# Optimization experiments

Hardware: AMD Instinct MI355X
Metric: run time of the kernel (lower is better)

Reference implementation:

```python
import jax, jax.numpy as jnp
import numpy as np

TAU = 0.1
SIGMA = 0.2
EPS = 1e-08
NUM_BINS = 128
IN_FEATURES = 512
OUT_FEATURES = 128
N = 4096
C = 16


def setup_inputs() -> dict:
    key = jax.random.key(0)
    ks = jax.random.split(key, 8)
    x1 = jax.random.normal(ks[0], (N, IN_FEATURES), dtype=jnp.float32)
    x2 = jax.random.normal(ks[1], (N, IN_FEATURES), dtype=jnp.float32)
    y1 = jax.random.randint(ks[2], (N,), 0, C, dtype=jnp.int32)
    y2 = jax.random.randint(ks[3], (N,), 0, C, dtype=jnp.int32)
    W1 = jax.random.normal(ks[4], (IN_FEATURES, OUT_FEATURES), dtype=jnp.float32) * 0.02
    b1 = jnp.zeros((OUT_FEATURES,), dtype=jnp.float32)
    W2 = jax.random.normal(ks[5], (OUT_FEATURES, OUT_FEATURES), dtype=jnp.float32) * 0.02
    b2 = jnp.zeros((OUT_FEATURES,), dtype=jnp.float32)
    bins = jnp.linspace(-5.0, 5.0, NUM_BINS).astype(jnp.float32)
    return {"input_embeddings_1": x1, "y1": y1, "input_embeddings_2": x2, "y2": y2,
            "W1": W1, "b1": b1, "W2": W2, "b2": b2, "bins": bins, "num_classes": C}


def _marginal_pdf(x_norm, bins):
    # x_norm: (b, D) L2-normalized rows; bins: (num_bins,)
    # residuals: (b, D, num_bins) -- dominant memory-bound intermediate
    kernel = jnp.exp(-0.5 * ((x_norm[:, :, None] - bins[None, None, :]) / SIGMA) ** 2)
    pdf = kernel.mean(axis=1)                         # (b, num_bins)
    pdf = pdf / (pdf.sum(axis=1, keepdims=True) + EPS)
    return jax.nn.softmax(pdf, axis=-1)


def _get_distribution(x, y, bins, num_classes):
    # x: (b, out_features) projected embeddings
    x_norm = x / jnp.linalg.norm(x, axis=1, keepdims=True)
    pdf = _marginal_pdf(x_norm, bins)                 # (b, num_bins)
    sums = jax.ops.segment_sum(pdf, y, num_segments=num_classes)
    counts = jax.ops.segment_sum(jnp.ones((y.shape[0],), pdf.dtype), y, num_segments=num_classes)
    return sums / counts[:, None]                     # (C, num_bins) per-class mean pdf


def _kld_matrix(A, M):
    P = jnp.concatenate([A, M], axis=0)               # (2C, num_bins)
    logP = jnp.log(P)
    inter = jnp.sum(P[:, None, :] * (logP[:, None, :] - logP[None, :, :]), axis=-1)
    n = P.shape[0]
    return inter * (1.0 - jnp.eye(n, dtype=P.dtype))


def reference(input_embeddings_1, y1, input_embeddings_2, y2, W1, b1, W2, b2, bins, num_classes):
    def proj(x):
        h = jax.nn.relu(x @ W1 + b1)
        return h @ W2 + b2

    dA = _get_distribution(proj(input_embeddings_1), y1, bins, num_classes)
    dB = _get_distribution(proj(input_embeddings_2), y2, bins, num_classes)
    M = 0.5 * (dA + dB)
    J = 0.5 * (_kld_matrix(dA, M) + _kld_matrix(dB, M))  # (2C, 2C)
    div_ij = jnp.diagonal(J, offset=num_classes)
    div_ji = jnp.diagonal(J, offset=-num_classes)
    positives = jnp.concatenate([div_ij, div_ji], axis=0)
    nominator = jnp.exp(positives / TAU)
    denominator = jnp.sum(jnp.exp(J / TAU), axis=1)
    partial_loss = -jnp.log(nominator / denominator)
    return jnp.mean(partial_loss)
```

## Files before the change

### kernel.cpp

```cpp
#include <hip/hip_runtime.h>
#include <hip/hip_bf16.h>

#define NROWS 4096
#define IN_F 512
#define OUT_F 128
#define NBINS 128
#define NCLS 16
#define EPSV 1e-8f
#define TAUV 0.1f
#define PSTRIDE (NCLS * NBINS + 32)

#define C2EXP (-18.0336880f)
#define INV_STEP (12.7f)
#define WRAD 17

#if defined(__has_builtin)
#if __has_builtin(__builtin_amdgcn_exp2f)
#define EXP2F(x) __builtin_amdgcn_exp2f(x)
#else
#define EXP2F(x) exp2f(x)
#endif
#else
#define EXP2F(x) exp2f(x)
#endif

typedef __attribute__((ext_vector_type(8))) short bf16x8;
typedef __attribute__((ext_vector_type(4))) float f32x4;

__device__ __forceinline__ short cvt_bf16(float x) {
    __hip_bfloat16 h = __float2bfloat16(x);
    return *reinterpret_cast<short*>(&h);
}

__global__ __launch_bounds__(128) void prep_w(
    const float* __restrict__ W1, const float* __restrict__ W2,
    __hip_bfloat16* __restrict__ W1T, __hip_bfloat16* __restrict__ W2T)
{
    const int n = blockIdx.x;
    const int t = threadIdx.x;
    for (int k = t; k < IN_F; k += 128)
        W1T[(size_t)n * IN_F + k] = __float2bfloat16(W1[(size_t)k * OUT_F + n]);
    W2T[(size_t)n * OUT_F + t] = __float2bfloat16(W2[(size_t)t * OUT_F + n]);
}

__global__ __launch_bounds__(512) void fused_proj_pdf(
    const float* __restrict__ X1, const float* __restrict__ X2,
    const int* __restrict__ Y1, const int* __restrict__ Y2,
    const __hip_bfloat16* __restrict__ W1T, const float* __restrict__ b1,
    const __hip_bfloat16* __restrict__ W2T, const float* __restrict__ b2,
    const float* __restrict__ bins,
    float* __restrict__ partial, float* __restrict__ pcnt)
{
    __shared__ __hip_bfloat16 xb[16][IN_F + 8];
    __shared__ __hip_bfloat16 h_lds[16][136];
    __shared__ float pout[16][128];
    __shared__ float rowX[8][2][128];
    __shared__ float smrows[16][128];
    __shared__ float bins_s[NBINS];
    __shared__ int   labs[16];
    const int tid  = threadIdx.x;
    const int wave = tid >> 6;
    const int lane = tid & 63;
    const int lr   = lane & 15;
    const int kg   = lane >> 4;
    const int row0 = blockIdx.x * 16;
    const int batch = (row0 < NROWS) ? 0 : 1;
    const float* __restrict__ X = batch ? X2 : X1;
    const int* __restrict__ Y = batch ? Y2 : Y1;
    const int xr0 = batch ? row0 - NROWS : row0;
    const int col = wave * 16 + lr;

    if (tid < NBINS) bins_s[tid] = bins[tid];
    if (tid >= 128 && tid < 144) labs[tid - 128] = Y[xr0 + tid - 128];

    for (int i = tid; i < 16 * 128; i += 512) {
        const int r = i >> 7, c4 = i & 127;
        float4 v = *reinterpret_cast<const float4*>(
            X + (size_t)(xr0 + r) * IN_F + c4 * 4);
        short4 s;
        s.x = cvt_bf16(v.x); s.y = cvt_bf16(v.y);
        s.z = cvt_bf16(v.z); s.w = cvt_bf16(v.w);
        *reinterpret_cast<short4*>(&xb[r][c4 * 4]) = s;
    }
    __syncthreads();

    f32x4 acc = {0.f, 0.f, 0.f, 0.f};
    {
        const __hip_bfloat16* __restrict__ wrow = W1T + (size_t)col * IN_F;
        #pragma unroll 4
        for (int ks = 0; ks < IN_F / 32; ++ks) {
            const int kb = ks * 32 + kg * 8;
            bf16x8 a = *reinterpret_cast<const bf16x8*>(&xb[lr][kb]);
            bf16x8 b = *reinterpret_cast<const bf16x8*>(wrow + kb);
            acc = __builtin_amdgcn_mfma_f32_16x16x32_bf16(a, b, acc, 0, 0, 0);
        }
    }
    {
        const float bb = b1[col];
        #pragma unroll
        for (int q = 0; q < 4; ++q)
            h_lds[kg * 4 + q][col] = __float2bfloat16(fmaxf(acc[q] + bb, 0.f));
    }
    __syncthreads();

    f32x4 c2 = {0.f, 0.f, 0.f, 0.f};
    {
        const __hip_bfloat16* __restrict__ w2row = W2T + (size_t)col * OUT_F;
        #pragma unroll
        for (int ks = 0; ks < OUT_F / 32; ++ks) {
            const int kb = ks * 32 + kg * 8;
            bf16x8 a2 = *reinterpret_cast<const bf16x8*>(&h_lds[lr][kb]);
            bf16x8 b2f = *reinterpret_cast<const bf16x8*>(w2row + kb);
            c2 = __builtin_amdgcn_mfma_f32_16x16x32_bf16(a2, b2f, c2, 0, 0, 0);
        }
    }
    {
        const float cb = b2[col];
        #pragma unroll
        for (int q = 0; q < 4; ++q)
            pout[kg * 4 + q][col] = c2[q] + cb;
    }
    __syncthreads();

    const int m0 = wave * 2, m1 = m0 + 1;

    const float p00 = pout[m0][lane], p01 = pout[m0][lane + 64];
    const float p10 = pout[m1][lane], p11 = pout[m1][lane + 64];

    float s0 = p00 * p00 + p01 * p01;
    float s1 = p10 * p10 + p11 * p11;
    #pragma unroll
    for (int off = 32; off; off >>= 1) {
        s0 += __shfl_xor(s0, off);
        s1 += __shfl_xor(s1, off);
    }
    const float i0 = __frsqrt_rn(s0), i1 = __frsqrt_rn(s1);
    const float x00 = p00 * i0, x01 = p01 * i0;
    const float x10 = p10 * i1, x11 = p11 * i1;

    rowX[wave][0][lane]      = x00;
    rowX[wave][0][lane + 64] = x01;
    rowX[wave][1][lane]      = x10;
    rowX[wave][1][lane + 64] = x11;

    float xlo = fminf(fminf(x00, x01), fminf(x10, x11));
    float xhi = fmaxf(fmaxf(x00, x01), fmaxf(x10, x11));
    #pragma unroll
    for (int off = 32; off; off >>= 1) {
        xlo = fminf(xlo, __shfl_xor(xlo, off));
        xhi = fmaxf(xhi, __shfl_xor(xhi, off));
    }
    int imin = (int)floorf((xlo + 5.0f) * INV_STEP) - WRAD;
    int imax = (int)ceilf ((xhi + 5.0f) * INV_STEP) + WRAD;
    imin = imin < 0 ? 0 : (imin > 127 ? 127 : imin);
    imax = imax > 127 ? 127 : (imax < 0 ? 0 : imax);
    if (imax > imin + 63) imax = imin + 63;
    const int nact = imax - imin + 1;
    const int j = imin + lane;
    const bool act = (j <= imax);
    const float bj = bins_s[act ? j : imax];

    const float4* __restrict__ x0v = reinterpret_cast<const float4*>(&rowX[wave][0][0]);
    const float4* __restrict__ x1v = reinterpret_cast<const float4*>(&rowX[wave][1][0]);
    float aA0 = 0.f, aA1 = 0.f, aB0 = 0.f, aB1 = 0.f;
    #pragma unroll 4
    for (int q = 0; q < 32; ++q) {
        float4 u = x0v[q];
        float4 v = x1v[q];
        float t;
        t = u.x - bj; aA0 += EXP2F((C2EXP * t) * t);
        t = u.z - bj; aA1 += EXP2F((C2EXP * t) * t);
        t = v.x - bj; aB0 += EXP2F((C2EXP * t) * t);
        t = v.z - bj; aB1 += EXP2F((C2EXP * t) * t);
        t = u.y - bj; aA0 += EXP2F((C2EXP * t) * t);
        t = u.w - bj; aA1 += EXP2F((C2EXP * t) * t);
        t = v.y - bj; aB0 += EXP2F((C2EXP * t) * t);
        t = v.w - bj; aB1 += EXP2F((C2EXP * t) * t);
    }
    float pdf0 = act ? (aA0 + aA1) * (1.0f / OUT_F) : 0.f;
    float pdf1 = act ? (aB0 + aB1) * (1.0f / OUT_F) : 0.f;

    float t0 = pdf0, t1 = pdf1;
    #pragma unroll
    for (int off = 32; off; off >>= 1) {
        t0 += __shfl_xor(t0, off);
        t1 += __shfl_xor(t1, off);
    }
    pdf0 *= 1.0f / (t0 + EPSV);
    pdf1 *= 1.0f / (t1 + EPSV);

    float mx0 = pdf0, mx1 = pdf1;
    #pragma unroll
    for (int off = 32; off; off >>= 1) {
        mx0 = fmaxf(mx0, __shfl_xor(mx0, off));
        mx1 = fmaxf(mx1, __shfl_xor(mx1, off));
    }
    const float q0 = act ? __expf(pdf0 - mx0) : 0.f;
    const float q1 = act ? __expf(pdf1 - mx1) : 0.f;
    const float ez0 = __expf(-mx0), ez1 = __expf(-mx1);
    float es0 = q0, es1 = q1;
    #pragma unroll
    for (int off = 32; off; off >>= 1) {
        es0 += __shfl_xor(es0, off);
        es1 += __shfl_xor(es1, off);
    }
    es0 += (float)(NBINS - nact) * ez0;
    es1 += (float)(NBINS - nact) * ez1;
    const float r0 = 1.0f / es0, r1 = 1.0f / es1;
    const float z0 = ez0 * r0, z1 = ez1 * r1;

    const int sa = lane - imin;
    const int sb = lane + 64 - imin;
    const float w0a = __shfl(q0, sa & 63) * r0;
    const float w0b = __shfl(q0, sb & 63) * r0;
    const float w1a = __shfl(q1, sa & 63) * r1;
    const float w1b = __shfl(q1, sb & 63) * r1;
    const bool ina = (unsigned)sa < (unsigned)nact;
    const bool inb = (unsigned)sb < (unsigned)nact;

    smrows[m0][lane]      = ina ? w0a : z0;
    smrows[m0][lane + 64] = inb ? w0b : z0;
    smrows[m1][lane]      = ina ? w1a : z1;
    smrows[m1][lane + 64] = inb ? w1b : z1;
    __syncthreads();

    {
        const int c_cls = tid >> 5;
        const int jq    = tid & 31;
        f32x4 accp = {0.f, 0.f, 0.f, 0.f};
        int ccnt = 0;
        #pragma unroll 4
        for (int r = 0; r < 16; ++r) {
            const float4 v = *reinterpret_cast<const float4*>(&smrows[r][jq * 4]);
            const float h = (labs[r] == c_cls) ? 1.f : 0.f;
            accp.x = fmaf(h, v.x, accp.x);
            accp.y = fmaf(h, v.y, accp.y);
            accp.z = fmaf(h, v.z, accp.z);
            accp.w = fmaf(h, v.w, accp.w);
            ccnt += (labs[r] == c_cls);
        }
        *reinterpret_cast<f32x4*>(
            &partial[(size_t)blockIdx.x * PSTRIDE + c_cls * NBINS + jq * 4]) = accp;
        if (jq == 0) pcnt[(size_t)blockIdx.x * NCLS + c_cls] = (float)ccnt;
    }
}

__global__ __launch_bounds__(256) void merge_kernel(
    const float* __restrict__ partial, const float* __restrict__ pcnt,
    float* __restrict__ dist, float* __restrict__ cntg)
{
    __shared__ float sd[16][17];
    __shared__ float sc[4];
    const int b = blockIdx.x;
    const int bc = b >> 3, jg = b & 7;
    const int batch = bc >> 4, c = bc & 15;
    const int j0 = jg * 16;
    const int tid = threadIdx.x;
    const int jl = tid & 15, s = tid >> 4;

    float acc = 0.f;
    #pragma unroll 4
    for (int k = 0; k < 16; ++k) {
        const int sb = s + k * 16;
        acc += partial[(size_t)(batch * 256 + sb) * PSTRIDE + c * NBINS + j0 + jl];
    }
    sd[s][jl] = acc;

    float cv = pcnt[(size_t)(batch * 256 + tid) * NCLS + c];
    #pragma unroll
    for (int off = 32; off; off >>= 1) cv += __shfl_xor(cv, off);
    if ((tid & 63) == 0) sc[tid >> 6] = cv;
    __syncthreads();

    if (tid < 16) {
        float d = 0.f;
        #pragma unroll
        for (int q = 0; q < 16; ++q) d += sd[q][tid];
        dist[(size_t)bc * NBINS + j0 + tid] = d;
    }
    if (jg == 0 && tid == 0) cntg[bc] = sc[0] + sc[1] + sc[2] + sc[3];
}

__global__ __launch_bounds__(512) void final_kernel(
    const float* __restrict__ dist, const float* __restrict__ cntg,
    float* __restrict__ out)
{
    __shared__ float P_A[32][132], L_A[32][132];
    __shared__ float P_B[32][132], L_B[32][132];
    __shared__ float JA[32][32], JB[32][32];
    __shared__ float pls[32];
    __shared__ float cnt[32];
    __shared__ float HA[32], HB[32];
    const int tid = threadIdx.x;

    if (tid < 32) cnt[tid] = cntg[tid];
    __syncthreads();

    for (int s = tid; s < NCLS * NBINS; s += 512) {
        const int c = s >> 7, jj = s & 127;
        const float a = dist[(size_t)c * NBINS + jj] / cnt[c];
        const float b = dist[(size_t)(16 + c) * NBINS + jj] / cnt[16 + c];
        const float mm = 0.5f * (a + b);
        const float lm = __logf(mm);
        P_A[c][jj] = a;        L_A[c][jj] = __logf(a);
        P_A[c + 16][jj] = mm;  L_A[c + 16][jj] = lm;
        P_B[c][jj] = b;        L_B[c][jj] = __logf(b);
        P_B[c + 16][jj] = mm;  L_B[c + 16][jj] = lm;
    }
    __syncthreads();

    if (tid < 64) {
        const int i = tid & 31;
        const float4* Pv = reinterpret_cast<const float4*>(
            (tid < 32) ? &P_A[i][0] : &P_B[i][0]);
        const float4* Lv = reinterpret_cast<const float4*>(
            (tid < 32) ? &L_A[i][0] : &L_B[i][0]);
        float h = 0.f;
        #pragma unroll 4
        for (int q = 0; q < 32; ++q) {
            float4 p = Pv[q], l = Lv[q];
            h = fmaf(p.x, l.x, h); h = fmaf(p.y, l.y, h);
            h = fmaf(p.z, l.z, h); h = fmaf(p.w, l.w, h);
        }
        if (tid < 32) HA[i] = h; else HB[i] = h;
    }
    __syncthreads();

    if (tid < 128) {
        const int side = tid >> 6;
        const int t = tid & 63;
        const int i0 = (t >> 3) << 2, k0 = (t & 7) << 2;
        const float4* pr[4];
        const float4* lq[4];
        #pragma unroll
        for (int a = 0; a < 4; ++a) {
            pr[a] = reinterpret_cast<const float4*>(
                side ? &P_B[i0 + a][0] : &P_A[i0 + a][0]);
            lq[a] = reinterpret_cast<const float4*>(
                side ? &L_B[k0 + a][0] : &L_A[k0 + a][0]);
        }
        float accv[4][4];
        #pragma unroll
        for (int a = 0; a < 4; ++a)
            #pragma unroll
            for (int b = 0; b < 4; ++b) accv[a][b] = 0.f;
        for (int q = 0; q < 32; ++q) {
            float4 Pv[4], Lv[4];
            #pragma unroll
            for (int a = 0; a < 4; ++a) { Pv[a] = pr[a][q]; Lv[a] = lq[a][q]; }
            #pragma unroll
            for (int a = 0; a < 4; ++a)
                #pragma unroll
                for (int b = 0; b < 4; ++b) {
                    accv[a][b] = fmaf(Pv[a].x, Lv[b].x, accv[a][b]);
                    accv[a][b] = fmaf(Pv[a].y, Lv[b].y, accv[a][b]);
                    accv[a][b] = fmaf(Pv[a].z, Lv[b].z, accv[a][b]);
                    accv[a][b] = fmaf(Pv[a].w, Lv[b].w, accv[a][b]);
                }
        }
        float (*Jout)[32] = side ? JB : JA;
        #pragma unroll
        for (int a = 0; a < 4; ++a)
            #pragma unroll
            for (int b = 0; b < 4; ++b)
                Jout[i0 + a][k0 + b] = accv[a][b];
    }
    __syncthreads();

    for (int p = tid; p < 32 * 32; p += 512) {
        const int i = p >> 5, k = p & 31;
        const float Jv = (i == k) ? 0.f
            : 0.5f * ((HA[i] - JA[i][k]) + (HB[i] - JB[i][k]));
        JA[i][k] = Jv;
    }
    __syncthreads();

    if (tid < 32) {
        float den = 0.f;
        for (int k = 0; k < 32; ++k) den += __expf(JA[tid][k] * (1.0f / TAUV));
        const float pos = JA[tid][(tid + 16) & 31];
        pls[tid] = -(pos * (1.0f / TAUV)) + __logf(den);
    }
    __syncthreads();
    if (tid == 0) {
        float s = 0.f;
        for (int i = 0; i < 32; ++i) s += pls[i];
        out[0] = s * (1.0f / 32.0f);
    }
}

extern "C" void kernel_launch(void* const* d_in, const int* in_sizes, int n_in,
                              void* d_out, int out_size, void* d_ws, size_t ws_size,
                              hipStream_t stream)
{
    const float* x1   = (const float*)d_in[0];
    const int*   y1   = (const int*)d_in[1];
    const float* x2   = (const float*)d_in[2];
    const int*   y2   = (const int*)d_in[3];
    const float* W1   = (const float*)d_in[4];
    const float* b1   = (const float*)d_in[5];
    const float* W2   = (const float*)d_in[6];
    const float* b2   = (const float*)d_in[7];
    const float* bins = (const float*)d_in[8];
    float* out = (float*)d_out;

    char* ws = (char*)d_ws;
    float* partial = (float*)ws;
    float* pcnt    = partial + (size_t)512 * PSTRIDE;
    float* dist    = pcnt + 512 * NCLS;
    float* cntg    = dist + 32 * NBINS;
    __hip_bfloat16* W1T = (__hip_bfloat16*)(cntg + 64);
    __hip_bfloat16* W2T = W1T + (size_t)OUT_F * IN_F;

    prep_w<<<128, 128, 0, stream>>>(W1, W2, W1T, W2T);
    fused_proj_pdf<<<512, 512, 0, stream>>>(x1, x2, y1, y2, W1T, b1, W2T, b2,
                                            bins, partial, pcnt);
    merge_kernel<<<256, 256, 0, stream>>>(partial, pcnt, dist, cntg);
    final_kernel<<<1, 512, 0, stream>>>(dist, cntg, out);
}
```

Baseline: 47.56 us.

## Halve rows per block to double grid size and process one row per wave

Each fused projection/pdf block now handles 8 rows instead of 16, so 1024 blocks are launched and each wave computes the KDE histogram for a single row. MFMA tiles still cover 16 rows, so half of each MFMA's work is duplicated and discarded. The merge kernel is reshaped to reduce twice as many partial histograms, and the workspace grows accordingly. The aim is more parallelism and shorter per-block latency on the large CU count, at the cost of doubling W1/W2 reads across blocks and doubling the partial-sum traffic.

After: 56.83 us, median of 2. 19.5% more time.

```diff
diff --git a/kernel.cpp b/kernel.cpp
--- a/kernel.cpp
+++ b/kernel.cpp
@@ -51,29 +51,30 @@
     const float* __restrict__ bins,
     float* __restrict__ partial, float* __restrict__ pcnt)
 {
-    __shared__ __hip_bfloat16 xb[16][IN_F + 8];
-    __shared__ __hip_bfloat16 h_lds[16][136];
-    __shared__ float pout[16][128];
-    __shared__ float rowX[8][2][128];
-    __shared__ float smrows[16][128];
+    __shared__ __hip_bfloat16 xb[8][IN_F + 8];
+    __shared__ __hip_bfloat16 h_lds[8][136];
+    __shared__ float pout[8][128];
+    __shared__ float rowX[8][128];
+    __shared__ float smrows[8][128];
     __shared__ float bins_s[NBINS];
-    __shared__ int   labs[16];
+    __shared__ int   labs[8];
     const int tid  = threadIdx.x;
     const int wave = tid >> 6;
     const int lane = tid & 63;
     const int lr   = lane & 15;
     const int kg   = lane >> 4;
-    const int row0 = blockIdx.x * 16;
+    const int row0 = blockIdx.x * 8;
     const int batch = (row0 < NROWS) ? 0 : 1;
     const float* __restrict__ X = batch ? X2 : X1;
     const int* __restrict__ Y = batch ? Y2 : Y1;
-    const int xr0 = batch ? row0 - NROWS : row0;
+    const int xr0 = row0 & (NROWS - 1);
     const int col = wave * 16 + lr;
 
     if (tid < NBINS) bins_s[tid] = bins[tid];
-    if (tid >= 128 && tid < 144) labs[tid - 128] = Y[xr0 + tid - 128];
-
-    for (int i = tid; i < 16 * 128; i += 512) {
+    if (tid >= 128 && tid < 136) labs[tid - 128] = Y[xr0 + tid - 128];
+
+    #pragma unroll
+    for (int i = tid; i < 8 * 128; i += 512) {
         const int r = i >> 7, c4 = i & 127;
         float4 v = *reinterpret_cast<const float4*>(
             X + (size_t)(xr0 + r) * IN_F + c4 * 4);
@@ -90,7 +91,7 @@
         #pragma unroll 4
         for (int ks = 0; ks < IN_F / 32; ++ks) {
             const int kb = ks * 32 + kg * 8;
-            bf16x8 a = *reinterpret_cast<const bf16x8*>(&xb[lr][kb]);
+            bf16x8 a = *reinterpret_cast<const bf16x8*>(&xb[lr & 7][kb]);
             bf16x8 b = *reinterpret_cast<const bf16x8*>(wrow + kb);
             acc = __builtin_amdgcn_mfma_f32_16x16x32_bf16(a, b, acc, 0, 0, 0);
         }
@@ -98,8 +99,11 @@
     {
         const float bb = b1[col];
         #pragma unroll
-        for (int q = 0; q < 4; ++q)
-            h_lds[kg * 4 + q][col] = __float2bfloat16(fmaxf(acc[q] + bb, 0.f));
+        for (int q = 0; q < 4; ++q) {
+            const int m = kg * 4 + q;
+            if (m < 8)
+                h_lds[m][col] = __float2bfloat16(fmaxf(acc[q] + bb, 0.f));
+        }
     }
     __syncthreads();
 
@@ -109,7 +113,7 @@
         #pragma unroll
         for (int ks = 0; ks < OUT_F / 32; ++ks) {
             const int kb = ks * 32 + kg * 8;
-            bf16x8 a2 = *reinterpret_cast<const bf16x8*>(&h_lds[lr][kb]);
+            bf16x8 a2 = *reinterpret_cast<const bf16x8*>(&h_lds[lr & 7][kb]);
             bf16x8 b2f = *reinterpret_cast<const bf16x8*>(w2row + kb);
             c2 = __builtin_amdgcn_mfma_f32_16x16x32_bf16(a2, b2f, c2, 0, 0, 0);
         }
@@ -117,34 +121,29 @@
     {
         const float cb = b2[col];
         #pragma unroll
-        for (int q = 0; q < 4; ++q)
-            pout[kg * 4 + q][col] = c2[q] + cb;
-    }
-    __syncthreads();
-
-    const int m0 = wave * 2, m1 = m0 + 1;
-
-    const float p00 = pout[m0][lane], p01 = pout[m0][lane + 64];
-    const float p10 = pout[m1][lane], p11 = pout[m1][lane + 64];
-
-    float s0 = p00 * p00 + p01 * p01;
-    float s1 = p10 * p10 + p11 * p11;
-    #pragma unroll
-    for (int off = 32; off; off >>= 1) {
-        s0 += __shfl_xor(s0, off);
-        s1 += __shfl_xor(s1, off);
-    }
-    const float i0 = __frsqrt_rn(s0), i1 = __frsqrt_rn(s1);
-    const float x00 = p00 * i0, x01 = p01 * i0;
-    const float x10 = p10 * i1, x11 = p11 * i1;
-
-    rowX[wave][0][lane]      = x00;
-    rowX[wave][0][lane + 64] = x01;
-    rowX[wave][1][lane]      = x10;
-    rowX[wave][1][lane + 64] = x11;
-
-    float xlo = fminf(fminf(x00, x01), fminf(x10, x11));
-    float xhi = fmaxf(fmaxf(x00, x01), fmaxf(x10, x11));
+        for (int q = 0; q < 4; ++q) {
+            const int m = kg * 4 + q;
+            if (m < 8)
+                pout[m][col] = c2[q] + cb;
+        }
+    }
+    __syncthreads();
+
+    const int m = wave;
+
+    const float p0 = pout[m][lane], p1 = pout[m][lane + 64];
+
+    float ss = p0 * p0 + p1 * p1;
+    #pragma unroll
+    for (int off = 32; off; off >>= 1) ss += __shfl_xor(ss, off);
+    const float inv = __frsqrt_rn(ss);
+    const float x0 = p0 * inv, x1 = p1 * inv;
+
+    rowX[m][lane]      = x0;
+    rowX[m][lane + 64] = x1;
+
+    float xlo = fminf(x0, x1);
+    float xhi = fmaxf(x0, x1);
     #pragma unroll
     for (int off = 32; off; off >>= 1) {
         xlo = fminf(xlo, __shfl_xor(xlo, off));
@@ -160,68 +159,45 @@
     const bool act = (j <= imax);
     const float bj = bins_s[act ? j : imax];
 
-    const float4* __restrict__ x0v = reinterpret_cast<const float4*>(&rowX[wave][0][0]);
-    const float4* __restrict__ x1v = reinterpret_cast<const float4*>(&rowX[wave][1][0]);
-    float aA0 = 0.f, aA1 = 0.f, aB0 = 0.f, aB1 = 0.f;
+    const float4* __restrict__ xv = reinterpret_cast<const float4*>(&rowX[m][0]);
+    float a0 = 0.f, a1 = 0.f;
     #pragma unroll 4
     for (int q = 0; q < 32; ++q) {
-        float4 u = x0v[q];
-        float4 v = x1v[q];
+        float4 u = xv[q];
         float t;
-        t = u.x - bj; aA0 += EXP2F((C2EXP * t) * t);
-        t = u.z - bj; aA1 += EXP2F((C2EXP * t) * t);
-        t = v.x - bj; aB0 += EXP2F((C2EXP * t) * t);
-        t = v.z - bj; aB1 += EXP2F((C2EXP * t) * t);
-        t = u.y - bj; aA0 += EXP2F((C2EXP * t) * t);
-        t = u.w - bj; aA1 += EXP2F((C2EXP * t) * t);
-        t = v.y - bj; aB0 += EXP2F((C2EXP * t) * t);
-        t = v.w - bj; aB1 += EXP2F((C2EXP * t) * t);
-    }
-    float pdf0 = act ? (aA0 + aA1) * (1.0f / OUT_F) : 0.f;
-    float pdf1 = act ? (aB0 + aB1) * (1.0f / OUT_F) : 0.f;
-
-    float t0 = pdf0, t1 = pdf1;
-    #pragma unroll
-    for (int off = 32; off; off >>= 1) {
-        t0 += __shfl_xor(t0, off);
-        t1 += __shfl_xor(t1, off);
-    }
-    pdf0 *= 1.0f / (t0 + EPSV);
-    pdf1 *= 1.0f / (t1 + EPSV);
-
-    float mx0 = pdf0, mx1 = pdf1;
-    #pragma unroll
-    for (int off = 32; off; off >>= 1) {
-        mx0 = fmaxf(mx0, __shfl_xor(mx0, off));
-        mx1 = fmaxf(mx1, __shfl_xor(mx1, off));
-    }
-    const float q0 = act ? __expf(pdf0 - mx0) : 0.f;
-    const float q1 = act ? __expf(pdf1 - mx1) : 0.f;
-    const float ez0 = __expf(-mx0), ez1 = __expf(-mx1);
-    float es0 = q0, es1 = q1;
-    #pragma unroll
-    for (int off = 32; off; off >>= 1) {
-        es0 += __shfl_xor(es0, off);
-        es1 += __shfl_xor(es1, off);
-    }
-    es0 += (float)(NBINS - nact) * ez0;
-    es1 += (float)(NBINS - nact) * ez1;
-    const float r0 = 1.0f / es0, r1 = 1.0f / es1;
-    const float z0 = ez0 * r0, z1 = ez1 * r1;
+        t = u.x - bj; a0 += EXP2F((C2EXP * t) * t);
+        t = u.z - bj; a1 += EXP2F((C2EXP * t) * t);
+        t = u.y - bj; a0 += EXP2F((C2EXP * t) * t);
+        t = u.w - bj; a1 += EXP2F((C2EXP * t) * t);
+    }
+    float pdf = act ? (a0 + a1) * (1.0f / OUT_F) : 0.f;
+
+    float ts = pdf;
+    #pragma unroll
+    for (int off = 32; off; off >>= 1) ts += __shfl_xor(ts, off);
+    pdf *= 1.0f / (ts + EPSV);
+
+    float mx = pdf;
+    #pragma unroll
+    for (int off = 32; off; off >>= 1) mx = fmaxf(mx, __shfl_xor(mx, off));
+    const float qv = act ? __expf(pdf - mx) : 0.f;
+    const float ez = __expf(-mx);
+    float es = qv;
+    #pragma unroll
+    for (int off = 32; off; off >>= 1) es += __shfl_xor(es, off);
+    es += (float)(NBINS - nact) * ez;
+    const float rcp = 1.0f / es;
+    const float z = ez * rcp;
 
     const int sa = lane - imin;
     const int sb = lane + 64 - imin;
-    const float w0a = __shfl(q0, sa & 63) * r0;
-    const float w0b = __shfl(q0, sb & 63) * r0;
-    const float w1a = __shfl(q1, sa & 63) * r1;
-    const float w1b = __shfl(q1, sb & 63) * r1;
+    const float wa = __shfl(qv, sa & 63) * rcp;
+    const float wb = __shfl(qv, sb & 63) * rcp;
     const bool ina = (unsigned)sa < (unsigned)nact;
     const bool inb = (unsigned)sb < (unsigned)nact;
 
-    smrows[m0][lane]      = ina ? w0a : z0;
-    smrows[m0][lane + 64] = inb ? w0b : z0;
-    smrows[m1][lane]      = ina ? w1a : z1;
-    smrows[m1][lane + 64] = inb ? w1b : z1;
+    smrows[m][lane]      = ina ? wa : z;
+    smrows[m][lane + 64] = inb ? wb : z;
     __syncthreads();
 
     {
@@ -229,8 +205,8 @@
         const int jq    = tid & 31;
         f32x4 accp = {0.f, 0.f, 0.f, 0.f};
         int ccnt = 0;
-        #pragma unroll 4
-        for (int r = 0; r < 16; ++r) {
+        #pragma unroll
+        for (int r = 0; r < 8; ++r) {
             const float4 v = *reinterpret_cast<const float4*>(&smrows[r][jq * 4]);
             const float h = (labs[r] == c_cls) ? 1.f : 0.f;
             accp.x = fmaf(h, v.x, accp.x);
@@ -249,33 +225,36 @@
     const float* __restrict__ partial, const float* __restrict__ pcnt,
     float* __restrict__ dist, float* __restrict__ cntg)
 {
-    __shared__ float sd[16][17];
+    __shared__ float sd[32][9];
     __shared__ float sc[4];
     const int b = blockIdx.x;
-    const int bc = b >> 3, jg = b & 7;
+    const int bc = b >> 4, jg = b & 15;
     const int batch = bc >> 4, c = bc & 15;
-    const int j0 = jg * 16;
+    const int j0 = jg * 8;
     const int tid = threadIdx.x;
-    const int jl = tid & 15, s = tid >> 4;
+    const int jl = tid & 7, s = tid >> 3;
 
     float acc = 0.f;
     #pragma unroll 4
     for (int k = 0; k < 16; ++k) {
-        const int sb = s + k * 16;
-        acc += partial[(size_t)(batch * 256 + sb) * PSTRIDE + c * NBINS + j0 + jl];
+        const int sb = s + k * 32;
+        acc += partial[(size_t)(batch * 512 + sb) * PSTRIDE + c * NBINS + j0 + jl];
     }
     sd[s][jl] = acc;
 
-    float cv = pcnt[(size_t)(batch * 256 + tid) * NCLS + c];
-    #pragma unroll
-    for (int off = 32; off; off >>= 1) cv += __shfl_xor(cv, off);
-    if ((tid & 63) == 0) sc[tid >> 6] = cv;
-    __syncthreads();
-
-    if (tid < 16) {
+    if (jg == 0) {
+        float cv = pcnt[(size_t)(batch * 512 + tid) * NCLS + c]
+                 + pcnt[(size_t)(batch * 512 + 256 + tid) * NCLS + c];
+        #pragma unroll
+        for (int off = 32; off; off >>= 1) cv += __shfl_xor(cv, off);
+        if ((tid & 63) == 0) sc[tid >> 6] = cv;
+    }
+    __syncthreads();
+
+    if (tid < 8) {
         float d = 0.f;
         #pragma unroll
-        for (int q = 0; q < 16; ++q) d += sd[q][tid];
+        for (int q = 0; q < 32; ++q) d += sd[q][tid];
         dist[(size_t)bc * NBINS + j0 + tid] = d;
     }
     if (jg == 0 && tid == 0) cntg[bc] = sc[0] + sc[1] + sc[2] + sc[3];
@@ -406,15 +385,15 @@
 
     char* ws = (char*)d_ws;
     float* partial = (float*)ws;
-    float* pcnt    = partial + (size_t)512 * PSTRIDE;
-    float* dist    = pcnt + 512 * NCLS;
+    float* pcnt    = partial + (size_t)1024 * PSTRIDE;
+    float* dist    = pcnt + 1024 * NCLS;
     float* cntg    = dist + 32 * NBINS;
     __hip_bfloat16* W1T = (__hip_bfloat16*)(cntg + 64);
     __hip_bfloat16* W2T = W1T + (size_t)OUT_F * IN_F;
 
     prep_w<<<128, 128, 0, stream>>>(W1, W2, W1T, W2T);
-    fused_proj_pdf<<<512, 512, 0, stream>>>(x1, x2, y1, y2, W1T, b1, W2T, b2,
-                                            bins, partial, pcnt);
-    merge_kernel<<<256, 256, 0, stream>>>(partial, pcnt, dist, cntg);
+    fused_proj_pdf<<<1024, 512, 0, stream>>>(x1, x2, y1, y2, W1T, b1, W2T, b2,
+                                             bins, partial, pcnt);
+    merge_kernel<<<512, 256, 0, stream>>>(partial, pcnt, dist, cntg);
     final_kernel<<<1, 512, 0, stream>>>(dist, cntg, out);
 }
```
